# Optimization experiments

Hardware: AMD Instinct MI355X
Metric: run time of the kernel (lower is better)

The kernel has to match this reference:

```python
import jax, jax.numpy as jnp
import numpy as np

HEAD_NUM = 16
H_DIM = 1024
Q_DIM = K_DIM = V_DIM = 1024
B, S = 16, 4096


def setup_inputs() -> dict:
    key = jax.random.key(0)
    ks = jax.random.split(key, 12)
    sc = lambda d: 1.0 / np.sqrt(d)
    return {
        "query": jax.random.normal(ks[0], (B, 1, Q_DIM), dtype=jnp.float32),
        "key_": jax.random.normal(ks[1], (B, S, K_DIM), dtype=jnp.float32),
        "value": jax.random.normal(ks[2], (B, S, V_DIM), dtype=jnp.float32),
        "Wq": jax.random.normal(ks[3], (H_DIM, Q_DIM), dtype=jnp.float32) * sc(Q_DIM),
        "bq": jnp.zeros((H_DIM,), jnp.float32),
        "Wk": jax.random.normal(ks[4], (H_DIM, K_DIM), dtype=jnp.float32) * sc(K_DIM),
        "bk": jnp.zeros((H_DIM,), jnp.float32),
        "Wv": jax.random.normal(ks[5], (H_DIM, V_DIM), dtype=jnp.float32) * sc(V_DIM),
        "bv": jnp.zeros((H_DIM,), jnp.float32),
        "Wf": jax.random.normal(ks[6], (H_DIM, H_DIM), dtype=jnp.float32) * sc(H_DIM),
        "bf": jnpp if False else jnp.zeros((H_DIM,), jnp.float32),
    }


def reference(query, key_, value, Wq, bq, Wk, bk, Wv, bv, Wf, bf):
    b, s, _ = key_.shape
    hd = H_DIM // HEAD_NUM
    # linear projections then split heads
    q = (query @ Wq.T + bq).reshape(b, 1, HEAD_NUM, hd)   # [B,1,H,D]
    k = (key_ @ Wk.T + bk).reshape(b, s, HEAD_NUM, hd)    # [B,S,H,D]
    v = (value @ Wv.T + bv).reshape(b, s, HEAD_NUM, hd)   # [B,S,H,D]
    # elementwise mul + reduce over head_dim -> [B,S,H]
    scores = jnp.sum(q * k, axis=-1) / jnp.sqrt(jnp.float32(H_DIM))
    # softmax over HEADS (dim=-1), faithful to the source
    att = jax.nn.softmax(scores, axis=-1)                 # [B,S,H]
    # weighted sum over seq_len -> [B,H,D]
    out = jnp.sum(att[..., None] * v, axis=1)
    out = out.reshape(b, 1, H_DIM)
    return out @ Wf.T + bf
```

## Files before the change

### kernel.cpp

```cpp
#include <hip/hip_runtime.h>
#include <math.h>

#define HEADS 16
#define HDIM 1024
#define NB 16
#define SEQ 4096
#define SCH 128
#define NCH (SEQ / SCH)
#define INV_SQRT 0.03125f

__device__ __forceinline__ float reduce16_to_lane(const float p[16], int lane) {
  float r8[8];
#pragma unroll
  for (int i = 0; i < 8; ++i) {
    float send = (lane & 16) ? p[i] : p[i + 8];
    float recv = __shfl_xor(send, 16, 64);
    r8[i] = ((lane & 16) ? p[i + 8] : p[i]) + recv;
  }
  float r4[4];
#pragma unroll
  for (int i = 0; i < 4; ++i) {
    float send = (lane & 8) ? r8[i] : r8[i + 4];
    float recv = __shfl_xor(send, 8, 64);
    r4[i] = ((lane & 8) ? r8[i + 4] : r8[i]) + recv;
  }
  float r2[2];
#pragma unroll
  for (int i = 0; i < 2; ++i) {
    float send = (lane & 4) ? r2[0] * 0.f + ((lane & 4) ? r4[i] : r4[i + 2]) : r4[i + 2];
    send = (lane & 4) ? r4[i] : r4[i + 2];
    float recv = __shfl_xor(send, 4, 64);
    r2[i] = ((lane & 4) ? r4[i + 2] : r4[i]) + recv;
  }
  float send = (lane & 2) ? r2[0] : r2[1];
  float recv = __shfl_xor(send, 2, 64);
  float x = ((lane & 2) ? r2[1] : r2[0]) + recv;
  x += __shfl_xor(x, 1, 64);
  x += __shfl_xor(x, 32, 64);
  return x;
}

__global__ __launch_bounds__(256) void k1_qproj(
    const float* __restrict__ query, const float* __restrict__ Wq,
    const float* __restrict__ bq, float* __restrict__ qout) {
  __shared__ __align__(16) float qlds[NB * HDIM];
  int t = threadIdx.x;
#pragma unroll
  for (int p = 0; p < 16; ++p)
    ((float4*)qlds)[t + p * 256] = ((const float4*)query)[t + p * 256];
  __syncthreads();
  int lane = t & 63, wave = t >> 6;
  int i = blockIdx.x * 4 + wave;
  float p_[NB];
#pragma unroll
  for (int b = 0; b < NB; ++b) p_[b] = 0.f;
#pragma unroll
  for (int it = 0; it < 4; ++it) {
    int j = it * 256 + lane * 4;
    float4 w4 = *(const float4*)(Wq + (size_t)i * HDIM + j);
#pragma unroll
    for (int b = 0; b < NB; ++b) {
      float4 q4 = *(const float4*)(qlds + b * HDIM + j);
      p_[b] += w4.x * q4.x + w4.y * q4.y + w4.z * q4.z + w4.w * q4.w;
    }
  }
  float x = reduce16_to_lane(p_, lane);
  if (lane < 32 && !(lane & 1)) {
    int b = lane >> 1;
    qout[b * HDIM + i] = x + bq[i];
  }
}

__global__ __launch_bounds__(256) void k2_wproj(
    const float* __restrict__ q, const float* __restrict__ Wk,
    const float* __restrict__ bk, float* __restrict__ wqk,
    float* __restrict__ qbk) {
  int t = threadIdx.x;
  int h = blockIdx.x;
  if (h < HEADS) {
    __shared__ __align__(16) float qlds[NB * 64];
    {
      int b = t >> 4, d4 = (t & 15) * 4;
      *(float4*)(qlds + b * 64 + d4) =
          *(const float4*)(q + (size_t)b * HDIM + h * 64 + d4);
    }
    __syncthreads();
    float4 acc[NB];
#pragma unroll
    for (int b = 0; b < NB; ++b) acc[b] = make_float4(0.f, 0.f, 0.f, 0.f);
    for (int d = 0; d < 64; ++d) {
      float4 w4 = *(const float4*)(Wk + (size_t)(h * 64 + d) * HDIM + t * 4);
#pragma unroll
      for (int b = 0; b < NB; ++b) {
        float qv = qlds[b * 64 + d];
        acc[b].x += qv * w4.x;
        acc[b].y += qv * w4.y;
        acc[b].z += qv * w4.z;
        acc[b].w += qv * w4.w;
      }
    }
#pragma unroll
    for (int b = 0; b < NB; ++b) {
      float4 o = make_float4(acc[b].x * INV_SQRT, acc[b].y * INV_SQRT,
                             acc[b].z * INV_SQRT, acc[b].w * INV_SQRT);
      *(float4*)(wqk + (size_t)(b * HEADS + h) * HDIM + t * 4) = o;
    }
  } else {
    int b = t >> 4, hh = t & 15;
    float s = 0.f;
    for (int d = 0; d < 64; ++d)
      s += q[(size_t)b * HDIM + hh * 64 + d] * bk[hh * 64 + d];
    qbk[b * HEADS + hh] = s * INV_SQRT;
  }
}

__global__ __launch_bounds__(256, 2) void k3_attn(
    const float* __restrict__ key, const float* __restrict__ value,
    const float* __restrict__ wqk, const float* __restrict__ qbk,
    float* __restrict__ A_part, float* __restrict__ l_part) {
  int t = threadIdx.x;
  int lane = t & 63, wave = t >> 6;
  int b = blockIdx.x / NCH;
  int c = blockIdx.x % NCH;
  __shared__ __align__(16) float sp[2][4][16];

  float4 wq[HEADS];
#pragma unroll
  for (int h = 0; h < HEADS; ++h)
    wq[h] = *(const float4*)(wqk + (size_t)(b * HEADS + h) * HDIM + t * 4);
  float4 qb4[4];
#pragma unroll
  for (int hq = 0; hq < 4; ++hq)
    qb4[hq] = *(const float4*)(qbk + b * HEADS + hq * 4);

  float4 Aacc[HEADS];
#pragma unroll
  for (int h = 0; h < HEADS; ++h) Aacc[h] = make_float4(0.f, 0.f, 0.f, 0.f);
  float lacc[HEADS];
#pragma unroll
  for (int h = 0; h < HEADS; ++h) lacc[h] = 0.f;

  const float4* kptr =
      (const float4*)(key + ((size_t)b * SEQ + (size_t)c * SCH) * HDIM) + t;
  const float4* vptr =
      (const float4*)(value + ((size_t)b * SEQ + (size_t)c * SCH) * HDIM) + t;

  float4 kf0 = kptr[0], vf0 = vptr[0];
  float4 kf1 = kptr[256], vf1 = vptr[256];

  for (int s = 0; s < SCH; ++s) {
    float4 kc = kf0, vc = vf0;
    kf0 = kf1;
    vf0 = vf1;
    if (s + 2 < SCH) {
      kf1 = kptr[(size_t)(s + 2) * 256];
      vf1 = vptr[(size_t)(s + 2) * 256];
    }
    float p_[16];
#pragma unroll
    for (int h = 0; h < HEADS; ++h)
      p_[h] = kc.x * wq[h].x + kc.y * wq[h].y + kc.z * wq[h].z + kc.w * wq[h].w;
    float x = reduce16_to_lane(p_, lane);
    int buf = s & 1;
    if (lane < 32 && !(lane & 1)) sp[buf][wave][lane >> 1] = x;
    __syncthreads();
    float sc[16];
#pragma unroll
    for (int hq = 0; hq < 4; ++hq) {
      float4 a0 = *(const float4*)&sp[buf][0][hq * 4];
      float4 a1 = *(const float4*)&sp[buf][1][hq * 4];
      float4 a2 = *(const float4*)&sp[buf][2][hq * 4];
      float4 a3 = *(const float4*)&sp[buf][3][hq * 4];
      sc[hq * 4 + 0] = a0.x + a1.x + a2.x + a3.x + qb4[hq].x;
      sc[hq * 4 + 1] = a0.y + a1.y + a2.y + a3.y + qb4[hq].y;
      sc[hq * 4 + 2] = a0.z + a1.z + a2.z + a3.z + qb4[hq].z;
      sc[hq * 4 + 3] = a0.w + a1.w + a2.w + a3.w + qb4[hq].w;
    }
    float e[16];
#pragma unroll
    for (int h = 0; h < HEADS; ++h) e[h] = __expf(sc[h]);
    float s01 = e[0] + e[1], s23 = e[2] + e[3], s45 = e[4] + e[5],
          s67 = e[6] + e[7], s89 = e[8] + e[9], sab = e[10] + e[11],
          scd = e[12] + e[13], sef = e[14] + e[15];
    float sum = ((s01 + s23) + (s45 + s67)) + ((s89 + sab) + (scd + sef));
    float rinv = 1.0f / sum;
#pragma unroll
    for (int h = 0; h < HEADS; ++h) {
      float a = e[h] * rinv;
      lacc[h] += a;
      Aacc[h].x += a * vc.x;
      Aacc[h].y += a * vc.y;
      Aacc[h].z += a * vc.z;
      Aacc[h].w += a * vc.w;
    }
  }
  size_t base = (size_t)(b * NCH + c) * HEADS * HDIM;
#pragma unroll
  for (int h = 0; h < HEADS; ++h)
    *(float4*)(A_part + base + (size_t)h * HDIM + t * 4) = Aacc[h];
  if (t == 0) {
#pragma unroll
    for (int h = 0; h < HEADS; ++h)
      l_part[(b * NCH + c) * HEADS + h] = lacc[h];
  }
}

__global__ __launch_bounds__(256) void k4_vproj(
    const float* __restrict__ A_part, const float* __restrict__ l_part,
    const float* __restrict__ Wv, const float* __restrict__ bv,
    float* __restrict__ o1) {
  __shared__ __align__(16) float Alds[HDIM];
  __shared__ float llds;
  int t = threadIdx.x;
  int b = blockIdx.x >> 4, h = blockIdx.x & 15;
  float4 a = make_float4(0.f, 0.f, 0.f, 0.f);
  for (int cc = 0; cc < NCH; ++cc) {
    float4 v = *(const float4*)(A_part +
                                ((size_t)(b * NCH + cc) * HEADS + h) * HDIM +
                                t * 4);
    a.x += v.x;
    a.y += v.y;
    a.z += v.z;
    a.w += v.w;
  }
  *(float4*)(Alds + t * 4) = a;
  if (t < 32) {
    float lv = l_part[(b * NCH + t) * HEADS + h];
    lv += __shfl_xor(lv, 1, 64);
    lv += __shfl_xor(lv, 2, 64);
    lv += __shfl_xor(lv, 4, 64);
    lv += __shfl_xor(lv, 8, 64);
    lv += __shfl_xor(lv, 16, 64);
    if (t == 0) llds = lv;
  }
  __syncthreads();
  int lane = t & 63, wave = t >> 6;
  float lval = llds;
#pragma unroll
  for (int p = 0; p < 16; ++p) {
    int d = p * 4 + wave;
    float acc = 0.f;
#pragma unroll
    for (int it = 0; it < 4; ++it) {
      int j = it * 256 + lane * 4;
      float4 w4 = *(const float4*)(Wv + (size_t)(h * 64 + d) * HDIM + j);
      float4 a4 = *(const float4*)(Alds + j);
      acc += w4.x * a4.x + w4.y * a4.y + w4.z * a4.z + w4.w * a4.w;
    }
    acc += __shfl_xor(acc, 1, 64);
    acc += __shfl_xor(acc, 2, 64);
    acc += __shfl_xor(acc, 4, 64);
    acc += __shfl_xor(acc, 8, 64);
    acc += __shfl_xor(acc, 16, 64);
    acc += __shfl_xor(acc, 32, 64);
    if (lane == 0)
      o1[(size_t)b * HDIM + h * 64 + d] = acc + lval * bv[h * 64 + d];
  }
}

__global__ __launch_bounds__(256) void k5_final(
    const float* __restrict__ o1, const float* __restrict__ Wf,
    const float* __restrict__ bf, float* __restrict__ out) {
  __shared__ __align__(16) float olds[NB * HDIM];
  int t = threadIdx.x;
#pragma unroll
  for (int p = 0; p < 16; ++p)
    ((float4*)olds)[t + p * 256] = ((const float4*)o1)[t + p * 256];
  __syncthreads();
  int lane = t & 63, wave = t >> 6;
  int i = blockIdx.x * 4 + wave;
  float p_[NB];
#pragma unroll
  for (int b = 0; b < NB; ++b) p_[b] = 0.f;
#pragma unroll
  for (int it = 0; it < 4; ++it) {
    int j = it * 256 + lane * 4;
    float4 w4 = *(const float4*)(Wf + (size_t)i * HDIM + j);
#pragma unroll
    for (int b = 0; b < NB; ++b) {
      float4 q4 = *(const float4*)(olds + b * HDIM + j);
      p_[b] += w4.x * q4.x + w4.y * q4.y + w4.z * q4.z + w4.w * q4.w;
    }
  }
  float x = reduce16_to_lane(p_, lane);
  if (lane < 32 && !(lane & 1)) {
    int bb = lane >> 1;
    out[(size_t)bb * HDIM + i] = x + bf[i];
  }
}

extern "C" void kernel_launch(void* const* d_in, const int* in_sizes, int n_in,
                              void* d_out, int out_size, void* d_ws,
                              size_t ws_size, hipStream_t stream) {
  const float* query = (const float*)d_in[0];
  const float* key_ = (const float*)d_in[1];
  const float* value = (const float*)d_in[2];
  const float* Wq = (const float*)d_in[3];
  const float* bq = (const float*)d_in[4];
  const float* Wk = (const float*)d_in[5];
  const float* bk = (const float*)d_in[6];
  const float* Wv = (const float*)d_in[7];
  const float* bv = (const float*)d_in[8];
  const float* Wf = (const float*)d_in[9];
  const float* bf = (const float*)d_in[10];
  float* out = (float*)d_out;

  float* ws = (float*)d_ws;
  float* wqk = ws;
  float* qbk = ws + 262144;
  float* qbuf = ws + 262400;
  float* o1 = ws + 278784;
  float* l_part = ws + 295168;
  float* A_part = ws + 303360;

  k1_qproj<<<256, 256, 0, stream>>>(query, Wq, bq, qbuf);
  k2_wproj<<<HEADS + 1, 256, 0, stream>>>(qbuf, Wk, bk, wqk, qbk);
  k3_attn<<<NB * NCH, 256, 0, stream>>>(key_, value, wqk, qbk, A_part, l_part);
  k4_vproj<<<NB * HEADS, 256, 0, stream>>>(A_part, l_part, Wv, bv, o1);
  k5_final<<<256, 256, 0, stream>>>(o1, Wf, bf, out);
}
```

Measured before the change: 679.1 us.

## Restructure attention kernel into LDS-tiled score phase and separate value phase

The attention kernel no longer does a per-row wave reduction with a block barrier on every sequence row. Each thread now owns one sequence row and computes its 16 head scores from LDS-transposed key tiles, reading the q·Wk weights as broadcasts. Softmax weights are written to LDS, and a second pass streams value rows with prefetching. The chunk size doubles, which halves the partials, and the wproj kernel is split across 256 blocks for more parallelism. The catch is that key and value are now read in separate phases, and the broadcast weight loads add heavy global/cache traffic.

Measured after the change: 1.014 ms. 1.49x slower.

```diff
diff --git a/kernel.cpp b/kernel.cpp
--- a/kernel.cpp
+++ b/kernel.cpp
@@ -5,9 +5,12 @@
 #define HDIM 1024
 #define NB 16
 #define SEQ 4096
-#define SCH 128
+#define SCH 256
 #define NCH (SEQ / SCH)
 #define INV_SQRT 0.03125f
+
+#define KT_STRIDE 68
+#define ATT_STRIDE 20
 
 __device__ __forceinline__ float reduce16_to_lane(const float p[16], int lane) {
   float r8[8];
@@ -27,8 +30,7 @@
   float r2[2];
 #pragma unroll
   for (int i = 0; i < 2; ++i) {
-    float send = (lane & 4) ? r2[0] * 0.f + ((lane & 4) ? r4[i] : r4[i + 2]) : r4[i + 2];
-    send = (lane & 4) ? r4[i] : r4[i + 2];
+    float send = (lane & 4) ? r4[i] : r4[i + 2];
     float recv = __shfl_xor(send, 4, 64);
     r2[i] = ((lane & 4) ? r4[i + 2] : r4[i]) + recv;
   }
@@ -75,133 +77,168 @@
     const float* __restrict__ q, const float* __restrict__ Wk,
     const float* __restrict__ bk, float* __restrict__ wqk,
     float* __restrict__ qbk) {
-  int t = threadIdx.x;
-  int h = blockIdx.x;
-  if (h < HEADS) {
-    __shared__ __align__(16) float qlds[NB * 64];
+  __shared__ __align__(16) float smem[17408];
+  int t = threadIdx.x;
+  int bid = blockIdx.x;
+  if (bid < 256) {
+    int h = bid >> 4, jb = bid & 15;
+    int j0 = jb * 64;
+    float* qlds = smem;
+    float4* plds = (float4*)(smem + 1024);
     {
-      int b = t >> 4, d4 = (t & 15) * 4;
-      *(float4*)(qlds + b * 64 + d4) =
-          *(const float4*)(q + (size_t)b * HDIM + h * 64 + d4);
-    }
-    __syncthreads();
-    float4 acc[NB];
-#pragma unroll
-    for (int b = 0; b < NB; ++b) acc[b] = make_float4(0.f, 0.f, 0.f, 0.f);
-    for (int d = 0; d < 64; ++d) {
-      float4 w4 = *(const float4*)(Wk + (size_t)(h * 64 + d) * HDIM + t * 4);
-#pragma unroll
-      for (int b = 0; b < NB; ++b) {
-        float qv = qlds[b * 64 + d];
-        acc[b].x += qv * w4.x;
-        acc[b].y += qv * w4.y;
-        acc[b].z += qv * w4.z;
-        acc[b].w += qv * w4.w;
+      int qb = t >> 4, qd = (t & 15) * 4;
+      *(float4*)&qlds[qb * 64 + qd] =
+          *(const float4*)(q + (size_t)qb * HDIM + h * 64 + qd);
+    }
+    __syncthreads();
+    int jq = t & 15, dg = t >> 4;
+    float4 acc[16];
+#pragma unroll
+    for (int bb = 0; bb < 16; ++bb) acc[bb] = make_float4(0.f, 0.f, 0.f, 0.f);
+#pragma unroll
+    for (int dd = 0; dd < 4; ++dd) {
+      int d = dg * 4 + dd;
+      float4 w4 = *(const float4*)(Wk + (size_t)(h * 64 + d) * HDIM + j0 + jq * 4);
+#pragma unroll
+      for (int bb = 0; bb < 16; ++bb) {
+        float qv = qlds[bb * 64 + d];
+        acc[bb].x += qv * w4.x;
+        acc[bb].y += qv * w4.y;
+        acc[bb].z += qv * w4.z;
+        acc[bb].w += qv * w4.w;
       }
     }
 #pragma unroll
-    for (int b = 0; b < NB; ++b) {
-      float4 o = make_float4(acc[b].x * INV_SQRT, acc[b].y * INV_SQRT,
-                             acc[b].z * INV_SQRT, acc[b].w * INV_SQRT);
-      *(float4*)(wqk + (size_t)(b * HEADS + h) * HDIM + t * 4) = o;
-    }
+    for (int bb = 0; bb < 16; ++bb) plds[dg * 256 + bb * 16 + jq] = acc[bb];
+    __syncthreads();
+    int obb = t >> 4, ojq = t & 15;
+    float4 s4 = make_float4(0.f, 0.f, 0.f, 0.f);
+#pragma unroll
+    for (int dg2 = 0; dg2 < 16; ++dg2) {
+      float4 v = plds[dg2 * 256 + obb * 16 + ojq];
+      s4.x += v.x; s4.y += v.y; s4.z += v.z; s4.w += v.w;
+    }
+    s4.x *= INV_SQRT; s4.y *= INV_SQRT; s4.z *= INV_SQRT; s4.w *= INV_SQRT;
+    *(float4*)(wqk + ((size_t)obb * HEADS + h) * HDIM + j0 + ojq * 4) = s4;
   } else {
+    float* qall = smem;
+    float* bkl = smem + 16384;
+#pragma unroll
+    for (int p = 0; p < 16; ++p)
+      ((float4*)qall)[t + p * 256] = ((const float4*)q)[t + p * 256];
+    ((float4*)bkl)[t] = ((const float4*)bk)[t];
+    __syncthreads();
     int b = t >> 4, hh = t & 15;
     float s = 0.f;
+#pragma unroll 8
     for (int d = 0; d < 64; ++d)
-      s += q[(size_t)b * HDIM + hh * 64 + d] * bk[hh * 64 + d];
+      s += qall[b * HDIM + hh * 64 + d] * bkl[hh * 64 + d];
     qbk[b * HEADS + hh] = s * INV_SQRT;
   }
 }
 
-__global__ __launch_bounds__(256, 2) void k3_attn(
+#define FMA4(A, c, v) \
+  { A.x += (c) * (v).x; A.y += (c) * (v).y; A.z += (c) * (v).z; A.w += (c) * (v).w; }
+
+__global__ __launch_bounds__(256) void k3_attn(
     const float* __restrict__ key, const float* __restrict__ value,
     const float* __restrict__ wqk, const float* __restrict__ qbk,
     float* __restrict__ A_part, float* __restrict__ l_part) {
-  int t = threadIdx.x;
-  int lane = t & 63, wave = t >> 6;
-  int b = blockIdx.x / NCH;
-  int c = blockIdx.x % NCH;
-  __shared__ __align__(16) float sp[2][4][16];
-
-  float4 wq[HEADS];
-#pragma unroll
-  for (int h = 0; h < HEADS; ++h)
-    wq[h] = *(const float4*)(wqk + (size_t)(b * HEADS + h) * HDIM + t * 4);
-  float4 qb4[4];
-#pragma unroll
-  for (int hq = 0; hq < 4; ++hq)
-    qb4[hq] = *(const float4*)(qbk + b * HEADS + hq * 4);
-
-  float4 Aacc[HEADS];
-#pragma unroll
-  for (int h = 0; h < HEADS; ++h) Aacc[h] = make_float4(0.f, 0.f, 0.f, 0.f);
-  float lacc[HEADS];
-#pragma unroll
-  for (int h = 0; h < HEADS; ++h) lacc[h] = 0.f;
-
-  const float4* kptr =
-      (const float4*)(key + ((size_t)b * SEQ + (size_t)c * SCH) * HDIM) + t;
-  const float4* vptr =
-      (const float4*)(value + ((size_t)b * SEQ + (size_t)c * SCH) * HDIM) + t;
-
-  float4 kf0 = kptr[0], vf0 = vptr[0];
-  float4 kf1 = kptr[256], vf1 = vptr[256];
-
-  for (int s = 0; s < SCH; ++s) {
-    float4 kc = kf0, vc = vf0;
-    kf0 = kf1;
-    vf0 = vf1;
-    if (s + 2 < SCH) {
-      kf1 = kptr[(size_t)(s + 2) * 256];
-      vf1 = vptr[(size_t)(s + 2) * 256];
-    }
-    float p_[16];
-#pragma unroll
-    for (int h = 0; h < HEADS; ++h)
-      p_[h] = kc.x * wq[h].x + kc.y * wq[h].y + kc.z * wq[h].z + kc.w * wq[h].w;
-    float x = reduce16_to_lane(p_, lane);
-    int buf = s & 1;
-    if (lane < 32 && !(lane & 1)) sp[buf][wave][lane >> 1] = x;
-    __syncthreads();
-    float sc[16];
-#pragma unroll
-    for (int hq = 0; hq < 4; ++hq) {
-      float4 a0 = *(const float4*)&sp[buf][0][hq * 4];
-      float4 a1 = *(const float4*)&sp[buf][1][hq * 4];
-      float4 a2 = *(const float4*)&sp[buf][2][hq * 4];
-      float4 a3 = *(const float4*)&sp[buf][3][hq * 4];
-      sc[hq * 4 + 0] = a0.x + a1.x + a2.x + a3.x + qb4[hq].x;
-      sc[hq * 4 + 1] = a0.y + a1.y + a2.y + a3.y + qb4[hq].y;
-      sc[hq * 4 + 2] = a0.z + a1.z + a2.z + a3.z + qb4[hq].z;
-      sc[hq * 4 + 3] = a0.w + a1.w + a2.w + a3.w + qb4[hq].w;
-    }
-    float e[16];
-#pragma unroll
-    for (int h = 0; h < HEADS; ++h) e[h] = __expf(sc[h]);
-    float s01 = e[0] + e[1], s23 = e[2] + e[3], s45 = e[4] + e[5],
-          s67 = e[6] + e[7], s89 = e[8] + e[9], sab = e[10] + e[11],
-          scd = e[12] + e[13], sef = e[14] + e[15];
-    float sum = ((s01 + s23) + (s45 + s67)) + ((s89 + sab) + (scd + sef));
-    float rinv = 1.0f / sum;
-#pragma unroll
-    for (int h = 0; h < HEADS; ++h) {
-      float a = e[h] * rinv;
-      lacc[h] += a;
-      Aacc[h].x += a * vc.x;
-      Aacc[h].y += a * vc.y;
-      Aacc[h].z += a * vc.z;
-      Aacc[h].w += a * vc.w;
-    }
-  }
-  size_t base = (size_t)(b * NCH + c) * HEADS * HDIM;
-#pragma unroll
-  for (int h = 0; h < HEADS; ++h)
-    *(float4*)(A_part + base + (size_t)h * HDIM + t * 4) = Aacc[h];
-  if (t == 0) {
-#pragma unroll
-    for (int h = 0; h < HEADS; ++h)
-      l_part[(b * NCH + c) * HEADS + h] = lacc[h];
+  __shared__ __align__(16) float kt[256 * KT_STRIDE];
+  __shared__ __align__(16) float att[256 * ATT_STRIDE];
+  int t = threadIdx.x;
+  int b = blockIdx.x >> 4;
+  int ch = blockIdx.x & 15;
+  int row0 = ch * SCH;
+  const float4* kg = (const float4*)(key + ((size_t)b * SEQ + row0) * HDIM);
+  const float* wqkb = wqk + (size_t)b * HEADS * HDIM;
+
+  float acc[16];
+#pragma unroll
+  for (int h = 0; h < 16; ++h) acc[h] = qbk[b * HEADS + h];
+
+  int pr = t >> 4, pc = t & 15;
+  float4 pf[16];
+#pragma unroll
+  for (int p = 0; p < 16; ++p) pf[p] = kg[(size_t)(p * 16 + pr) * 256 + pc];
+#pragma unroll
+  for (int p = 0; p < 16; ++p)
+    *(float4*)&kt[(p * 16 + pr) * KT_STRIDE + pc * 4] = pf[p];
+  __syncthreads();
+
+  for (int jt = 0; jt < 16; ++jt) {
+    if (jt < 15) {
+#pragma unroll
+      for (int p = 0; p < 16; ++p)
+        pf[p] = kg[(size_t)(p * 16 + pr) * 256 + (jt + 1) * 16 + pc];
+    }
+    const float* wjt = wqkb + jt * 64;
+#pragma unroll
+    for (int q = 0; q < 16; ++q) {
+      float4 k4 = *(const float4*)&kt[t * KT_STRIDE + q * 4];
+      const float* w = wjt + q * 4;
+#pragma unroll
+      for (int h = 0; h < 16; ++h) {
+        acc[h] += k4.x * w[h * HDIM] + k4.y * w[h * HDIM + 1] +
+                  k4.z * w[h * HDIM + 2] + k4.w * w[h * HDIM + 3];
+      }
+    }
+    __syncthreads();
+    if (jt < 15) {
+#pragma unroll
+      for (int p = 0; p < 16; ++p)
+        *(float4*)&kt[(p * 16 + pr) * KT_STRIDE + pc * 4] = pf[p];
+    }
+    __syncthreads();
+  }
+
+  float e[16];
+#pragma unroll
+  for (int h = 0; h < 16; ++h) e[h] = __expf(acc[h]);
+  float s01 = e[0] + e[1], s23 = e[2] + e[3], s45 = e[4] + e[5],
+        s67 = e[6] + e[7], s89 = e[8] + e[9], sab = e[10] + e[11],
+        scd = e[12] + e[13], sef = e[14] + e[15];
+  float sum = ((s01 + s23) + (s45 + s67)) + ((s89 + sab) + (scd + sef));
+  float rinv = 1.0f / sum;
+#pragma unroll
+  for (int h = 0; h < 16; ++h) att[t * ATT_STRIDE + h] = e[h] * rinv;
+  __syncthreads();
+
+  float4 Aacc[16];
+#pragma unroll
+  for (int h = 0; h < 16; ++h) Aacc[h] = make_float4(0.f, 0.f, 0.f, 0.f);
+  const float4* vg = (const float4*)(value + ((size_t)b * SEQ + row0) * HDIM) + t;
+  float4 vpf[8];
+#pragma unroll
+  for (int i = 0; i < 8; ++i) vpf[i] = vg[(size_t)i * 256];
+  for (int s8 = 0; s8 < 32; ++s8) {
+#pragma unroll
+    for (int i = 0; i < 8; ++i) {
+      int s = s8 * 8 + i;
+      float4 vc = vpf[i];
+      if (s8 < 31) vpf[i] = vg[(size_t)(s + 8) * 256];
+      float4 a0 = *(const float4*)&att[s * ATT_STRIDE];
+      float4 a1 = *(const float4*)&att[s * ATT_STRIDE + 4];
+      float4 a2 = *(const float4*)&att[s * ATT_STRIDE + 8];
+      float4 a3 = *(const float4*)&att[s * ATT_STRIDE + 12];
+      FMA4(Aacc[0], a0.x, vc); FMA4(Aacc[1], a0.y, vc);
+      FMA4(Aacc[2], a0.z, vc); FMA4(Aacc[3], a0.w, vc);
+      FMA4(Aacc[4], a1.x, vc); FMA4(Aacc[5], a1.y, vc);
+      FMA4(Aacc[6], a1.z, vc); FMA4(Aacc[7], a1.w, vc);
+      FMA4(Aacc[8], a2.x, vc); FMA4(Aacc[9], a2.y, vc);
+      FMA4(Aacc[10], a2.z, vc); FMA4(Aacc[11], a2.w, vc);
+      FMA4(Aacc[12], a3.x, vc); FMA4(Aacc[13], a3.y, vc);
+      FMA4(Aacc[14], a3.z, vc); FMA4(Aacc[15], a3.w, vc);
+    }
+  }
+  size_t abase = (size_t)(b * NCH + ch) * HEADS * HDIM;
+#pragma unroll
+  for (int h = 0; h < 16; ++h)
+    *(float4*)(A_part + abase + (size_t)h * HDIM + t * 4) = Aacc[h];
+  if (t < 16) {
+    float l = 0.f;
+    for (int s = 0; s < 256; ++s) l += att[s * ATT_STRIDE + t];
+    l_part[(b * NCH + ch) * HEADS + t] = l;
   }
 }
 
@@ -214,23 +251,20 @@
   int t = threadIdx.x;
   int b = blockIdx.x >> 4, h = blockIdx.x & 15;
   float4 a = make_float4(0.f, 0.f, 0.f, 0.f);
+#pragma unroll
   for (int cc = 0; cc < NCH; ++cc) {
     float4 v = *(const float4*)(A_part +
                                 ((size_t)(b * NCH + cc) * HEADS + h) * HDIM +
                                 t * 4);
-    a.x += v.x;
-    a.y += v.y;
-    a.z += v.z;
-    a.w += v.w;
-  }
-  *(float4*)(Alds + t * 4) = a;
-  if (t < 32) {
+    a.x += v.x; a.y += v.y; a.z += v.z; a.w += v.w;
+  }
+  *(float4*)&Alds[t * 4] = a;
+  if (t < 16) {
     float lv = l_part[(b * NCH + t) * HEADS + h];
     lv += __shfl_xor(lv, 1, 64);
     lv += __shfl_xor(lv, 2, 64);
     lv += __shfl_xor(lv, 4, 64);
     lv += __shfl_xor(lv, 8, 64);
-    lv += __shfl_xor(lv, 16, 64);
     if (t == 0) llds = lv;
   }
   __syncthreads();
@@ -311,10 +345,10 @@
   float* qbuf = ws + 262400;
   float* o1 = ws + 278784;
   float* l_part = ws + 295168;
-  float* A_part = ws + 303360;
+  float* A_part = ws + 299264;
 
   k1_qproj<<<256, 256, 0, stream>>>(query, Wq, bq, qbuf);
-  k2_wproj<<<HEADS + 1, 256, 0, stream>>>(qbuf, Wk, bk, wqk, qbk);
+  k2_wproj<<<257, 256, 0, stream>>>(qbuf, Wk, bk, wqk, qbk);
   k3_attn<<<NB * NCH, 256, 0, stream>>>(key_, value, wqk, qbk, A_part, l_part);
   k4_vproj<<<NB * HEADS, 256, 0, stream>>>(A_part, l_part, Wv, bv, o1);
   k5_final<<<256, 256, 0, stream>>>(o1, Wf, bf, out);
```
